# Kernel optimization log

Hardware: AMD Instinct MI355X
Metric: run time of the kernel (lower is better)

## Reference

```python
import jax, jax.numpy as jnp
import numpy as np
from jax import lax

B, DIM, H, W = 4, 256, 32, 32
NH = 8
HD = DIM // NH            # 32; CDA uses doubled head dim 2*HD=64
HIDDEN = 512              # FFN hidden, multiple of DIM (groups=DIM dwconv)
DEPTH = 1
LAMBDA_INIT = 0.8 - 0.6 * float(np.exp(-0.3 * DEPTH))
EPS = 1e-5


def conv1x1(w, x):
    # w: (out,in), x: (b,in,h,w)
    return jnp.einsum('oi,bihw->bohw', w, x)


def dwconv(x, w, groups):
    return lax.conv_general_dilated(x, w, (1, 1), 'SAME',
                                    dimension_numbers=('NCHW', 'OIHW', 'NCHW'),
                                    feature_group_count=groups)


def layernorm_c(x, wgt, bias):
    # WithBias LayerNorm over channel dim (to_3d -> LN(-1) -> to_4d)
    mu = jnp.mean(x, axis=1, keepdims=True)
    var = jnp.mean((x - mu) ** 2, axis=1, keepdims=True)
    return (x - mu) / jnp.sqrt(var + EPS) * wgt[None, :, None, None] + bias[None, :, None, None]


def batchnorm(x, g, b, m, v):
    return (x - m[None, :, None, None]) / jnp.sqrt(v[None, :, None, None] + EPS) \
        * g[None, :, None, None] + b[None, :, None, None]


def _cda(x, wq, wk, wv, lq1, lk1, lq2, lk2, rms_scale, wo):
    b, c, hh, ww = x.shape
    n = hh * ww

    def heads(wp):
        t = conv1x1(wp, x).reshape(b, NH, 2 * HD, n)
        return jnp.transpose(t, (0, 1, 3, 2))  # b h n (2hd)

    Q, K, V = heads(wq), heads(wk), heads(wv)
    scale = HD ** -0.5
    a1 = jax.nn.softmax(jnp.einsum('bhnd,bhmd->bhnm', Q[..., :HD], K[..., :HD]) * scale, axis=-1)
    a2 = jax.nn.softmax(jnp.einsum('bhnd,bhmd->bhnm', Q[..., HD:], K[..., HD:]) * scale, axis=-1)
    lam = jnp.exp(jnp.sum(lq1 * lk1, -1)) - jnp.exp(jnp.sum(lq2 * lk2, -1)) + LAMBDA_INIT  # (NH,)
    out = jnp.einsum('bhnm,bhmd->bhnd', a1 - lam[None, :, None, None] * a2, V)
    rms = jnp.sqrt(jnp.mean(out * out, axis=-1, keepdims=True) + EPS)
    out = out / rms * rms_scale * (1.0 - LAMBDA_INIT)
    out = jnp.transpose(out, (0, 1, 3, 2)).reshape(b, 2 * c, hh, ww)
    return conv1x1(wo, out)


def _cha(x, temp, wqkv, wdw, wout):
    b, c, hh, ww = x.shape
    n = hh * ww
    qkv = dwconv(conv1x1(wqkv, x), wdw, 3 * DIM)
    r = qkv.reshape(b, 3, NH, c // NH, n)
    q, k, v = r[:, 0], r[:, 1], r[:, 2]
    q = q / jnp.maximum(jnp.linalg.norm(q, axis=-1, keepdims=True), 1e-12)
    k = k / jnp.maximum(jnp.linalg.norm(k, axis=-1, keepdims=True), 1e-12)
    attn = jax.nn.softmax(jnp.einsum('bhcn,bhdn->bhcd', q, k) * temp[None, :, None, None], axis=-1)
    out = jnp.einsum('bhcd,bhdn->bhcn', attn, v).reshape(b, c, hh, ww)
    return conv1x1(wout, out)


def _ffn(x, bn1_g, bn1_b, bn1_m, bn1_v, w1, b1, bn2_g, bn2_b, bn2_m, bn2_v, w2, b2, w3, b3):
    h = batchnorm(x, bn1_g, bn1_b, bn1_m, bn1_v)
    h = conv1x1(w1, h) + b1[None, :, None, None]
    h = batchnorm(h, bn2_g, bn2_b, bn2_m, bn2_v)
    h = dwconv(h, w2, DIM) + b2[None, :, None, None]
    h = jnp.clip(h, 0.0, 6.0)  # ReLU6
    return conv1x1(w3, h) + b3[None, :, None, None]


def setup_inputs() -> dict:
    key = jax.random.key(0)
    ks = jax.random.split(key, 20)
    nrm = lambda i, shape, s=0.02: jax.random.normal(ks[i], shape, jnp.float32) * s
    return {
        'x': jax.random.normal(ks[0], (B, DIM, H, W), jnp.float32),
        'ln1_w': jnp.ones((DIM,), jnp.float32), 'ln1_b': jnp.zeros((DIM,), jnp.float32),
        'cda_wq': nrm(1, (2 * DIM, DIM)), 'cda_wk': nrm(2, (2 * DIM, DIM)), 'cda_wv': nrm(3, (2 * DIM, DIM)),
        'cda_lq1': nrm(4, (NH, HD), 0.1), 'cda_lk1': nrm(5, (NH, HD), 0.1),
        'cda_lq2': nrm(6, (NH, HD), 0.1), 'cda_lk2': nrm(7, (NH, HD), 0.1),
        'cda_rms_scale': jnp.ones((2 * HD,), jnp.float32), 'cda_wo': nrm(8, (DIM, 2 * DIM)),
        'ln2_w': jnp.ones((DIM,), jnp.float32), 'ln2_b': jnp.zeros((DIM,), jnp.float32),
        'cha_temp': jnp.ones((NH,), jnp.float32),
        'cha_wqkv': nrm(9, (3 * DIM, DIM)), 'cha_wdw': nrm(10, (3 * DIM, 1, 3, 3), 0.1),
        'cha_wout': nrm(11, (DIM, DIM)),
        'ln3_w': jnp.ones((DIM,), jnp.float32), 'ln3_b': jnp.zeros((DIM,), jnp.float32),
        'bn1_g': jnp.ones((DIM,), jnp.float32), 'bn1_b': jnp.zeros((DIM,), jnp.float32),
        'bn1_m': nrm(12, (DIM,), 0.1), 'bn1_v': jnp.ones((DIM,), jnp.float32),
        'ffn_w1': nrm(13, (HIDDEN, DIM)), 'ffn_b1': jnp.zeros((HIDDEN,), jnp.float32),
        'bn2_g': jnp.ones((HIDDEN,), jnp.float32), 'bn2_b': jnp.zeros((HIDDEN,), jnp.float32),
        'bn2_m': nrm(14, (HIDDEN,), 0.1), 'bn2_v': jnp.ones((HIDDEN,), jnp.float32),
        'ffn_w2': nrm(15, (HIDDEN, HIDDEN // DIM, 3, 3), 0.1), 'ffn_b2': jnp.zeros((HIDDEN,), jnp.float32),
        'ffn_w3': nrm(16, (DIM, HIDDEN)), 'ffn_b3': jnp.zeros((DIM,), jnp.float32),
    }


def reference(x, ln1_w, ln1_b, cda_wq, cda_wk, cda_wv, cda_lq1, cda_lk1, cda_lq2, cda_lk2,
              cda_rms_scale, cda_wo, ln2_w, ln2_b, cha_temp, cha_wqkv, cha_wdw, cha_wout,
              ln3_w, ln3_b, bn1_g, bn1_b, bn1_m, bn1_v, ffn_w1, ffn_b1, bn2_g, bn2_b,
              bn2_m, bn2_v, ffn_w2, ffn_b2, ffn_w3, ffn_b3):
    h = layernorm_c(x, ln1_w, ln1_b)
    x = x + _cda(h, cda_wq, cda_wk, cda_wv, cda_lq1, cda_lk1, cda_lq2, cda_lk2, cda_rms_scale, cda_wo)
    h = layernorm_c(x, ln2_w, ln2_b)
    x = x + _cha(h, cha_temp, cha_wqkv, cha_wdw, cha_wout)
    h = layernorm_c(x, ln3_w, ln3_b)
    x = x + _ffn(h, bn1_g, bn1_b, bn1_m, bn1_v, ffn_w1, ffn_b1, bn2_g, bn2_b, bn2_m, bn2_v, ffn_w2, ffn_b2, ffn_w3, ffn_b3)
    return x
```

## Files before the change

kernel.cpp:

```cpp
#include <hip/hip_runtime.h>
#include <hip/hip_bf16.h>

typedef __hip_bfloat16 bf16;
typedef __attribute__((ext_vector_type(8))) short s16x8;
typedef __attribute__((ext_vector_type(4))) float f32x4;

#define DEV __device__ __forceinline__

DEV float b2f(bf16 v){ return __bfloat162float(v); }
DEV ushort f2bf(float f){ bf16 h = __float2bfloat16(f); return *reinterpret_cast<ushort*>(&h); }

constexpr int NPIX = 1024;
constexpr float EPSF = 1e-5f;
constexpr float LAMBDA_INIT_F = 0.3555090675909693f;
constexpr float ONE_M_LI     = 0.6444909324090307f;
constexpr float ATT_SCALE    = 0.17677669529663687f;

constexpr size_t OFF_WBF   = 2120448;
constexpr size_t OFF_QT    = 2644736;
constexpr size_t OFF_V16   = 4741888;
constexpr size_t OFF_ATT   = 5790464;
constexpr size_t OFF_BUF1  = 6839040;
constexpr size_t OFF_BUF2  = 9984768;
constexpr size_t OFF_SPART = 13130496;
constexpr size_t OFF_STATS = 13425408;
constexpr size_t OFF_EFF   = 13449984;
constexpr size_t OFF_FLAG  = 13452608;

struct PackArgs { const void* p[34]; };

__global__ __launch_bounds__(256) void detect_kernel(const void* __restrict__ x, int* __restrict__ flag){
  __shared__ int sh;
  if (threadIdx.x == 0) sh = 0;
  __syncthreads();
  const bf16* h = (const bf16*)x;
  int local = 0;
  for (int i = threadIdx.x; i < 4096; i += 256){
    float v = b2f(h[i]);
    if (!(fabsf(v) <= 1e6f)) local = 1;
  }
  if (local) atomicOr(&sh, 1);
  __syncthreads();
  if (threadIdx.x == 0) *flag = sh;
}

DEV float rdin(const PackArgs& a, int i, int idx, int flag){
  return flag ? ((const float*)a.p[i])[idx] : b2f(((const bf16*)a.p[i])[idx]);
}

__global__ __launch_bounds__(256) void prep_all_kernel(PackArgs args, const int* __restrict__ flagp,
    float* __restrict__ P, ushort* __restrict__ W, float* __restrict__ eff){
  const int t = threadIdx.x;
  const int blk = blockIdx.x;
  const int flag = *flagp;
  if (blk < 8283){
    constexpr int NIN = 34;
    constexpr int off[NIN+1] = {0,1048576,1048832,1049088,1180160,1311232,1442304,1442560,
      1442816,1443072,1443328,1443392,1574464,1574720,1574976,1574984,1771592,1778504,
      1844040,1844296,1844552,1844808,1845064,1845320,1845576,1976648,1977160,1977672,
      1978184,1978696,1979208,1988424,1988936,2120008,2120264};
    const int g = blk*256 + t;
    if (g >= off[NIN]) return;
    int idx = 0;
    #pragma unroll
    for (int k = 1; k < NIN; k++) idx = (g >= off[k]) ? k : idx;
    P[g] = rdin(args, idx, g - off[idx], flag);
  } else if (blk < 9307){
    const int g = (blk - 8283)*1024 + t*4;
    int src, loc;
    if      (g <  131072){ src = 3;  loc = g; }
    else if (g <  262144){ src = 4;  loc = g - 131072; }
    else if (g <  393216){ src = 5;  loc = g - 262144; }
    else if (g <  589824){ src = 15; loc = g - 393216; }
    else if (g <  720896){ src = 11; loc = g - 589824; }
    else if (g <  786432){ src = 17; loc = g - 720896; }
    else if (g <  917504){ src = 24; loc = g - 786432; }
    else                 { src = 32; loc = g - 917504; }
    ushort4 o;
    if (flag){
      const float4 v = *(const float4*)((const float*)args.p[src] + loc);
      o = make_ushort4(f2bf(v.x), f2bf(v.y), f2bf(v.z), f2bf(v.w));
    } else {
      o = *(const ushort4*)((const ushort*)args.p[src] + loc);
    }
    *(ushort4*)&W[g] = o;
  } else {
    eff[t]      = rdin(args,1,t,flag);  eff[256+t] = rdin(args,2,t,flag);
    eff[512+t]  = rdin(args,12,t,flag); eff[768+t] = rdin(args,13,t,flag);
    const float s1 = rdin(args,20,t,flag) * rsqrtf(rdin(args,23,t,flag) + EPSF);
    eff[1024+t] = rdin(args,18,t,flag) * s1;
    eff[1280+t] = (rdin(args,19,t,flag) - rdin(args,22,t,flag)) * s1 + rdin(args,21,t,flag);
    for (int c = t; c < 512; c += 256){
      const float sc = rdin(args,26,c,flag) * rsqrtf(rdin(args,29,c,flag) + EPSF);
      eff[1536+c] = sc;
      eff[2048+c] = rdin(args,27,c,flag) - rdin(args,28,c,flag)*sc;
    }
    if (t < 8){
      float e1 = 0.f, e2 = 0.f;
      for (int i = 0; i < 32; i++){
        e1 += rdin(args,6,t*32+i,flag) * rdin(args,7,t*32+i,flag);
        e2 += rdin(args,8,t*32+i,flag) * rdin(args,9,t*32+i,flag);
      }
      eff[2560+t] = __expf(e1) - __expf(e2) + LAMBDA_INIT_F;
    }
  }
}

__global__ __launch_bounds__(256) void ln_stats_kernel(const float* __restrict__ x,
    float* __restrict__ mu, float* __restrict__ rstd){
  __shared__ float ps[16][64], ps2[16][64];
  const int t = threadIdx.x;
  const int b = blockIdx.x >> 4, n0 = (blockIdx.x & 15)*64;
  const int tn = t & 15, tc = t >> 4;
  float4 s = {0,0,0,0}, q = {0,0,0,0};
  #pragma unroll
  for (int i = 0; i < 16; i++){
    const int c = tc*16 + i;
    const float4 v = *(const float4*)&x[((size_t)b*256 + c)*NPIX + n0 + tn*4];
    s.x += v.x; s.y += v.y; s.z += v.z; s.w += v.w;
    q.x += v.x*v.x; q.y += v.y*v.y; q.z += v.z*v.z; q.w += v.w*v.w;
  }
  ps[tc][tn*4+0]=s.x; ps[tc][tn*4+1]=s.y; ps[tc][tn*4+2]=s.z; ps[tc][tn*4+3]=s.w;
  ps2[tc][tn*4+0]=q.x; ps2[tc][tn*4+1]=q.y; ps2[tc][tn*4+2]=q.z; ps2[tc][tn*4+3]=q.w;
  __syncthreads();
  if (t < 64){
    float a = 0.f, qq = 0.f;
    #pragma unroll
    for (int j = 0; j < 16; j++){ a += ps[j][t]; qq += ps2[j][t]; }
    const float m = a * (1.f/256.f);
    float var = qq * (1.f/256.f) - m*m; var = fmaxf(var, 0.f);
    mu[(size_t)b*NPIX + n0 + t] = m;
    rstd[(size_t)b*NPIX + n0 + t] = rsqrtf(var + EPSF);
  }
}

template<int INM, int EPIM, bool BIAS, bool BN2F>
__global__ __launch_bounds__(256) void gemm_kernel(
    const float* __restrict__ Xf, const ushort* __restrict__ Xb, const ushort* __restrict__ W,
    const float* __restrict__ bias, const float* __restrict__ mu, const float* __restrict__ rstd,
    const float* __restrict__ effw, const float* __restrict__ effb,
    const float* __restrict__ s2, const float* __restrict__ t2,
    const float* __restrict__ res, void* __restrict__ out,
    ushort* __restrict__ qt, ushort* __restrict__ v16,
    int Cin, const int* __restrict__ flag)
{
  __shared__ ushort Xt[64][72];
  const int t = threadIdx.x;
  const int nb = blockIdx.x*64, ob = blockIdx.y*64, b = blockIdx.z;
  const int lane = t & 63, w = t >> 6;
  const int wR = w >> 1, wC = w & 1;
  const int l15 = lane & 15, g = lane >> 4;
  const int tn = t & 63, tc4 = t >> 6;
  const f32x4 z4 = {0.f,0.f,0.f,0.f};
  f32x4 acc[2][2] = {{z4,z4},{z4,z4}};

  for (int kb = 0; kb < Cin; kb += 64){
    if (INM == 2){
      const ushort* src = Xb + ((size_t)b*NPIX + nb + tn)*Cin + kb + tc4*16;
      *(uint4*)&Xt[tn][tc4*16]   = *(const uint4*)src;
      *(uint4*)&Xt[tn][tc4*16+8] = *(const uint4*)(src+8);
    } else {
      float m_ = 0.f, r_ = 1.f;
      if (INM == 0){ m_ = mu[(size_t)b*NPIX + nb + tn]; r_ = rstd[(size_t)b*NPIX + nb + tn]; }
      ushort tmp[16];
      #pragma unroll
      for (int i = 0; i < 16; i++){
        const int c = kb + tc4*16 + i;
        float v = Xf[((size_t)b*Cin + c)*NPIX + nb + tn];
        if (INM == 0) v = (v - m_)*r_*effw[c] + effb[c];
        tmp[i] = f2bf(v);
      }
      *(uint4*)&Xt[tn][tc4*16]   = *(uint4*)&tmp[0];
      *(uint4*)&Xt[tn][tc4*16+8] = *(uint4*)&tmp[8];
    }
    __syncthreads();
    #pragma unroll
    for (int ks = 0; ks < 2; ks++){
      const s16x8 a0 = *(const s16x8*)&W[(size_t)(ob + wR*32 + l15)*Cin + kb + ks*32 + g*8];
      const s16x8 a1 = *(const s16x8*)&W[(size_t)(ob + wR*32 + 16 + l15)*Cin + kb + ks*32 + g*8];
      const s16x8 b0 = *(const s16x8*)&Xt[wC*32 + l15][ks*32 + g*8];
      const s16x8 b1 = *(const s16x8*)&Xt[wC*32 + 16 + l15][ks*32 + g*8];
      acc[0][0] = __builtin_amdgcn_mfma_f32_16x16x32_bf16(a0, b0, acc[0][0], 0,0,0);
      acc[0][1] = __builtin_amdgcn_mfma_f32_16x16x32_bf16(a0, b1, acc[0][1], 0,0,0);
      acc[1][0] = __builtin_amdgcn_mfma_f32_16x16x32_bf16(a1, b0, acc[1][0], 0,0,0);
      acc[1][1] = __builtin_amdgcn_mfma_f32_16x16x32_bf16(a1, b1, acc[1][1], 0,0,0);
    }
    __syncthreads();
  }

  const int Cout = gridDim.y*64;
  #pragma unroll
  for (int fr = 0; fr < 2; fr++){
    #pragma unroll
    for (int fc = 0; fc < 2; fc++){
      const int o = ob + wR*32 + fr*16 + 4*g;
      const int n = nb + wC*32 + fc*16 + l15;
      const f32x4 v = acc[fr][fc];
      if (EPIM == 0){
        if (ob < 1024){
          const int qk = o >> 9, h = (o >> 6) & 7, d = o & 63;
          ushort4 pk = make_ushort4(f2bf(v[0]), f2bf(v[1]), f2bf(v[2]), f2bf(v[3]));
          ushort* dst = qt + ((((size_t)qk*4 + b)*8 + h)*NPIX + n)*64 + d;
          *(ushort4*)dst = pk;
        } else {
          const int c = o - 1024;
          #pragma unroll
          for (int r = 0; r < 4; r++)
            v16[((size_t)b*512 + c + r)*NPIX + n] = f2bf(v[r]);
        }
      } else {
        #pragma unroll
        for (int r = 0; r < 4; r++){
          float val = v[r];
          if (BIAS) val += bias[o + r];
          if (BN2F) val = val*s2[o+r] + t2[o+r];
          const size_t row = ((size_t)b*Cout + o + r)*NPIX + n;
          if (EPIM == 1){ ((float*)out)[row] = val + res[row]; }
          else if (EPIM == 2){ ((float*)out)[row] = val; }
          else {
            val += res[row];
            if (*flag) ((float*)out)[row] = val;
            else       ((ushort*)out)[row] = f2bf(val);
          }
        }
      }
    }
  }
}

__global__ __launch_bounds__(256) void attn_kernel(
    const ushort* __restrict__ QT, const ushort* __restrict__ V16,
    const float* __restrict__ Pf, const float* __restrict__ lamArr,
    ushort* __restrict__ att)
{
  __shared__ ushort Ks[2][4096];
  __shared__ ushort Vs[2][4096];
  const int t = threadIdx.x;
  const int lane = t & 63, w = t >> 6;
  const int l15 = lane & 15, g = lane >> 4;
  const int qt = blockIdx.x, h = blockIdx.y, b = blockIdx.z;
  const int qsub = qt*64 + w*16;
  const ushort* Qb = QT + ((size_t)b*8 + h)*NPIX*64;
  const ushort* Kb = QT + ((size_t)(4 + b)*8 + h)*NPIX*64;
  const ushort* Vb = V16 + ((size_t)b*512 + h*64)*NPIX;

  const int c0row = t >> 3, c0col = t & 7;
  const int c1row = (t + 256) >> 3, c1col = t & 7;
  const int sw0 = (c0col ^ (c0row & 7))*8;
  const int sw1 = (c1col ^ (c1row & 7))*8;

  s16x8 bq[2];
  #pragma unroll
  for (int hx = 0; hx < 2; hx++)
    bq[hx] = *(const s16x8*)&Qb[(size_t)(qsub + l15)*64 + 32*hx + 8*g];
  const float lam = lamArr[h];

  const f32x4 z4 = {0.f,0.f,0.f,0.f};
  f32x4 o0[4] = {z4,z4,z4,z4};
  f32x4 o1[4] = {z4,z4,z4,z4};
  float z[2] = {0.f, 0.f};

  uint4 kra = *(const uint4*)&Kb[(size_t)c0row*64 + c0col*8];
  uint4 krb = *(const uint4*)&Kb[(size_t)c1row*64 + c1col*8];
  uint4 vra = *(const uint4*)&Vb[(size_t)c0row*NPIX + c0col*8];
  uint4 vrb = *(const uint4*)&Vb[(size_t)c1row*NPIX + c1col*8];
  *(uint4*)&Ks[0][c0row*64 + sw0] = kra;
  *(uint4*)&Ks[0][c1row*64 + sw1] = krb;
  *(uint4*)&Vs[0][c0row*64 + sw0] = vra;
  *(uint4*)&Vs[0][c1row*64 + sw1] = vrb;
  kra = *(const uint4*)&Kb[(size_t)(64 + c0row)*64 + c0col*8];
  krb = *(const uint4*)&Kb[(size_t)(64 + c1row)*64 + c1col*8];
  vra = *(const uint4*)&Vb[(size_t)c0row*NPIX + 64 + c0col*8];
  vrb = *(const uint4*)&Vb[(size_t)c1row*NPIX + 64 + c1col*8];
  __syncthreads();

  #pragma unroll 1
  for (int it = 0; it < 16; it++){
    const int cur = it & 1;
    const ushort* Kc = &Ks[cur][0];
    const ushort* Vc = &Vs[cur][0];

    f32x4 s[2][4];
    #pragma unroll
    for (int fr = 0; fr < 4; fr++){
      const int row = fr*16 + l15;
      const int rx = (row & 7)*8;
      #pragma unroll
      for (int hx = 0; hx < 2; hx++){
        const s16x8 ak = *(const s16x8*)&Kc[row*64 + ((hx*32 + 8*g) ^ rx)];
        s[hx][fr] = __builtin_amdgcn_mfma_f32_16x16x32_bf16(ak, bq[hx], z4, 0,0,0);
      }
    }
    s16x8 pa[2][2];
    #pragma unroll
    for (int hx = 0; hx < 2; hx++){
      #pragma unroll
      for (int ms = 0; ms < 2; ms++){
        ushort tmp[8];
        #pragma unroll
        for (int fr2 = 0; fr2 < 2; fr2++)
          #pragma unroll
          for (int r = 0; r < 4; r++){
            const float e = __expf(s[hx][ms*2 + fr2][r] * ATT_SCALE);
            z[hx] += e;
            tmp[fr2*4 + r] = f2bf(e);
          }
        pa[hx][ms] = *(s16x8*)tmp;
      }
    }
    __builtin_amdgcn_s_setprio(1);
    #pragma unroll
    for (int ms = 0; ms < 2; ms++){
      #pragma unroll
      for (int dc = 0; dc < 4; dc++){
        const int row = dc*16 + l15;
        const int r7 = row & 7;
        const int elo = ms*32 + 4*g;
        const int eloswz = ((((elo >> 3) ^ r7) << 3) | (elo & 7));
        const int ehi = elo + 16;
        const int ehiswz = ((((ehi >> 3) ^ r7) << 3) | (ehi & 7));
        const uint2 lo = *(const uint2*)&Vc[row*64 + eloswz];
        const uint2 hi = *(const uint2*)&Vc[row*64 + ehiswz];
        union { uint u[4]; s16x8 v; } bv;
        bv.u[0] = lo.x; bv.u[1] = lo.y; bv.u[2] = hi.x; bv.u[3] = hi.y;
        o0[dc] = __builtin_amdgcn_mfma_f32_16x16x32_bf16(pa[0][ms], bv.v, o0[dc], 0,0,0);
        o1[dc] = __builtin_amdgcn_mfma_f32_16x16x32_bf16(pa[1][ms], bv.v, o1[dc], 0,0,0);
      }
    }
    __builtin_amdgcn_s_setprio(0);

    if (it < 15){
      const int nxt = cur ^ 1;
      *(uint4*)&Ks[nxt][c0row*64 + sw0] = kra;
      *(uint4*)&Ks[nxt][c1row*64 + sw1] = krb;
      *(uint4*)&Vs[nxt][c0row*64 + sw0] = vra;
      *(uint4*)&Vs[nxt][c1row*64 + sw1] = vrb;
      if (it < 14){
        const int m0 = (it + 2)*64;
        kra = *(const uint4*)&Kb[(size_t)(m0 + c0row)*64 + c0col*8];
        krb = *(const uint4*)&Kb[(size_t)(m0 + c1row)*64 + c1col*8];
        vra = *(const uint4*)&Vb[(size_t)c0row*NPIX + m0 + c0col*8];
        vrb = *(const uint4*)&Vb[(size_t)c1row*NPIX + m0 + c1col*8];
      }
    }
    __syncthreads();
  }

  #pragma unroll
  for (int hx = 0; hx < 2; hx++){
    z[hx] += __shfl_xor(z[hx], 16);
    z[hx] += __shfl_xor(z[hx], 32);
  }
  float zi0[4], zi1[4];
  #pragma unroll
  for (int r = 0; r < 4; r++){
    zi0[r] = 1.f / __shfl(z[0], 4*g + r);
    zi1[r] = 1.f / __shfl(z[1], 4*g + r);
  }
  float val[4][4];
  float ss[4] = {0.f,0.f,0.f,0.f};
  #pragma unroll
  for (int dc = 0; dc < 4; dc++)
    #pragma unroll
    for (int r = 0; r < 4; r++){
      const float vv = o0[dc][r]*zi0[r] - lam*o1[dc][r]*zi1[r];
      val[dc][r] = vv; ss[r] += vv*vv;
    }
  #pragma unroll
  for (int r = 0; r < 4; r++){
    ss[r] += __shfl_xor(ss[r], 1);
    ss[r] += __shfl_xor(ss[r], 2);
    ss[r] += __shfl_xor(ss[r], 4);
    ss[r] += __shfl_xor(ss[r], 8);
  }
  float rinv[4];
  #pragma unroll
  for (int r = 0; r < 4; r++) rinv[r] = ONE_M_LI * rsqrtf(ss[r]*(1.f/64.f) + EPSF);
  #pragma unroll
  for (int dc = 0; dc < 4; dc++){
    const float rs = Pf[1443328 + dc*16 + l15];
    #pragma unroll
    for (int r = 0; r < 4; r++){
      const int n = qsub + 4*g + r;
      att[((size_t)b*NPIX + n)*512 + h*64 + dc*16 + l15] = f2bf(val[dc][r]*rinv[r]*rs);
    }
  }
}

__global__ __launch_bounds__(256) void dwl2_kernel(const float* __restrict__ in,
    const float* __restrict__ wdw, float* __restrict__ out){
  __shared__ float tile[1024];
  __shared__ float wsum[4];
  const int p = blockIdx.x;
  const int c = p % 768;
  const int t = threadIdx.x;
  const float* ip = in + (size_t)p*1024;
  *(float4*)&tile[t*4] = *(const float4*)&ip[t*4];
  float wv[9];
  #pragma unroll
  for (int i = 0; i < 9; i++) wv[i] = wdw[c*9+i];
  __syncthreads();
  float o[4]; float ssq = 0.f;
  #pragma unroll
  for (int j = 0; j < 4; j++){
    const int px = t*4 + j, x = px & 31, y = px >> 5;
    float s = 0.f;
    #pragma unroll
    for (int ky = 0; ky < 3; ky++){
      const int yy = y + ky - 1;
      if (yy < 0 || yy > 31) continue;
      #pragma unroll
      for (int kx = 0; kx < 3; kx++){
        const int xx = x + kx - 1;
        if (xx < 0 || xx > 31) continue;
        s = fmaf(tile[yy*32+xx], wv[ky*3+kx], s);
      }
    }
    o[j] = s; ssq += s*s;
  }
  for (int off = 32; off; off >>= 1) ssq += __shfl_down(ssq, off);
  if ((t & 63) == 0) wsum[t >> 6] = ssq;
  __syncthreads();
  float inv = 1.f;
  if (c < 512){
    const float tot = wsum[0]+wsum[1]+wsum[2]+wsum[3];
    inv = 1.f / fmaxf(sqrtf(tot), 1e-12f);
  }
  *(float4*)&out[(size_t)p*1024 + t*4] = make_float4(o[0]*inv, o[1]*inv, o[2]*inv, o[3]*inv);
}

__global__ __launch_bounds__(256) void cha_scores_kernel(const float* __restrict__ qk,
                                                         float* __restrict__ spart){
  __shared__ float qs[32][129];
  __shared__ float ks[32][129];
  const int t = threadIdx.x;
  const int nb = blockIdx.x*128;
  const int bh = blockIdx.y, b = bh >> 3, h = bh & 7;
  const size_t qbase = ((size_t)b*768 + h*32)*NPIX + nb;
  const size_t kbase = qbase + (size_t)256*NPIX;
  { const int c = t >> 3, n0 = (t & 7)*16;
    #pragma unroll
    for (int j = 0; j < 16; j++){
      qs[c][n0+j] = qk[qbase + (size_t)c*NPIX + n0 + j];
      ks[c][n0+j] = qk[kbase + (size_t)c*NPIX + n0 + j];
    } }
  __syncthreads();
  const int c = t & 31, dg = t >> 5;
  float acc[4] = {};
  for (int nn = 0; nn < 128; nn++){
    const float qv = qs[c][nn];
    #pragma unroll
    for (int j = 0; j < 4; j++) acc[j] = fmaf(qv, ks[dg*4+j][nn], acc[j]);
  }
  float* sp = spart + ((size_t)bh*8 + blockIdx.x)*1024 + c*32 + dg*4;
  #pragma unroll
  for (int j = 0; j < 4; j++) sp[j] = acc[j];
}

__global__ __launch_bounds__(256) void cha_pv_kernel(const float* __restrict__ spart,
    const float* __restrict__ tempP, const float* __restrict__ qkv, float* __restrict__ out){
  __shared__ float Ps[32][33];
  const int t = threadIdx.x;
  const int bh = blockIdx.y, b = bh >> 3, h = bh & 7;
  const int nb = blockIdx.x*64;
  const float tf = tempP[h];
  for (int p = t; p < 1024; p += 256){
    float s = 0.f;
    #pragma unroll
    for (int ch = 0; ch < 8; ch++) s += spart[((size_t)bh*8 + ch)*1024 + p];
    Ps[p >> 5][p & 31] = s * tf;
  }
  __syncthreads();
  if (t < 32){
    float mx = -1e30f;
    #pragma unroll
    for (int d = 0; d < 32; d++) mx = fmaxf(mx, Ps[t][d]);
    float sum = 0.f;
    float e[32];
    #pragma unroll
    for (int d = 0; d < 32; d++){ e[d] = __expf(Ps[t][d]-mx); sum += e[d]; }
    const float inv = 1.f/sum;
    #pragma unroll
    for (int d = 0; d < 32; d++) Ps[t][d] = e[d]*inv;
  }
  __syncthreads();
  const int n = nb + (t & 63);
  const int cg = t >> 6;
  const size_t vbase = ((size_t)b*768 + 512 + h*32)*NPIX + n;
  float acc[8] = {};
  for (int d = 0; d < 32; d++){
    const float v = qkv[vbase + (size_t)d*NPIX];
    #pragma unroll
    for (int j = 0; j < 8; j++) acc[j] = fmaf(Ps[cg*8+j][d], v, acc[j]);
  }
  const size_t obase = ((size_t)b*256 + h*32 + cg*8)*NPIX + n;
  #pragma unroll
  for (int j = 0; j < 8; j++) out[obase + (size_t)j*NPIX] = acc[j];
}

__global__ void gconv3_kernel(const float* __restrict__ in, const float* __restrict__ w,
                              const float* __restrict__ bias, float* __restrict__ out){
  const int gIdx = blockIdx.x*256 + threadIdx.x;
  const int x = gIdx & 31, y = (gIdx >> 5) & 31;
  const int plane = gIdx >> 10;
  const int o = plane & 511, b = plane >> 9;
  const float* ip = in + ((size_t)b*512 + (o & ~1))*NPIX;
  float s = bias[o];
  #pragma unroll
  for (int ci = 0; ci < 2; ci++){
    #pragma unroll
    for (int ky = 0; ky < 3; ky++){
      const int yy = y + ky - 1;
      if (yy < 0 || yy > 31) continue;
      #pragma unroll
      for (int kx = 0; kx < 3; kx++){
        const int xx = x + kx - 1;
        if (xx < 0 || xx > 31) continue;
        s = fmaf(ip[(size_t)ci*NPIX + yy*32+xx], w[o*18 + ci*9 + ky*3 + kx], s);
      }
    }
  }
  out[gIdx] = fminf(fmaxf(s, 0.f), 6.f);
}

extern "C" void kernel_launch(void* const* d_in, const int* in_sizes, int n_in,
                              void* d_out, int out_size, void* d_ws, size_t ws_size,
                              hipStream_t stream)
{
  (void)in_sizes; (void)n_in; (void)out_size; (void)ws_size;

  float* ws   = (float*)d_ws;
  float* P    = ws;
  float* xbuf = P;
  ushort* Wbf = (ushort*)(ws + OFF_WBF);
  ushort* QT  = (ushort*)(ws + OFF_QT);
  ushort* V16 = (ushort*)(ws + OFF_V16);
  ushort* att = (ushort*)(ws + OFF_ATT);
  float* chaout = ws + OFF_ATT;
  float* buf1 = ws + OFF_BUF1;
  float* buf2 = ws + OFF_BUF2;
  float* spart= ws + OFF_SPART;
  float* stats= ws + OFF_STATS;
  float* eff  = ws + OFF_EFF;
  int*  flag  = (int*)(ws + OFF_FLAG);

  const float* b1f = P + 1976648;
  const float* b3f = P + 2120008;
  const float* w2f = P + 1979208;
  const float* b2f_ = P + 1988424;
  const float* temp = P + 1574976;

  detect_kernel<<<1, 256, 0, stream>>>(d_in[0], flag);
  PackArgs pa;
  for (int i = 0; i < 34; i++) pa.p[i] = d_in[i];
  prep_all_kernel<<<9308, 256, 0, stream>>>(pa, flag, P, Wbf, eff);

  ln_stats_kernel<<<64, 256, 0, stream>>>(xbuf, stats, stats+4096);
  gemm_kernel<0,0,false,false><<<dim3(16,24,4), 256, 0, stream>>>(
      xbuf, nullptr, Wbf, nullptr, stats, stats+4096, eff, eff+256,
      nullptr, nullptr, nullptr, nullptr, QT, V16, 256, nullptr);
  attn_kernel<<<dim3(16,8,4), 256, 0, stream>>>(QT, V16, P, eff+2560, att);
  gemm_kernel<2,1,false,false><<<dim3(16,4,4), 256, 0, stream>>>(
      nullptr, att, Wbf+589824, nullptr, nullptr, nullptr, nullptr, nullptr,
      nullptr, nullptr, xbuf, xbuf, nullptr, nullptr, 512, nullptr);

  ln_stats_kernel<<<64, 256, 0, stream>>>(xbuf, stats+8192, stats+12288);
  gemm_kernel<0,2,false,false><<<dim3(16,12,4), 256, 0, stream>>>(
      xbuf, nullptr, Wbf+393216, nullptr, stats+8192, stats+12288, eff+512, eff+768,
      nullptr, nullptr, nullptr, buf1, nullptr, nullptr, 256, nullptr);
  dwl2_kernel<<<3072, 256, 0, stream>>>(buf1, P + 1771592, buf2);
  cha_scores_kernel<<<dim3(8,32), 256, 0, stream>>>(buf2, spart);
  cha_pv_kernel<<<dim3(16,32), 256, 0, stream>>>(spart, temp, buf2, chaout);
  gemm_kernel<1,1,false,false><<<dim3(16,4,4), 256, 0, stream>>>(
      chaout, nullptr, Wbf+720896, nullptr, nullptr, nullptr, nullptr, nullptr,
      nullptr, nullptr, xbuf, xbuf, nullptr, nullptr, 256, nullptr);

  ln_stats_kernel<<<64, 256, 0, stream>>>(xbuf, stats+16384, stats+20480);
  gemm_kernel<0,2,true,true><<<dim3(16,8,4), 256, 0, stream>>>(
      xbuf, nullptr, Wbf+786432, b1f, stats+16384, stats+20480, eff+1024, eff+1280,
      eff+1536, eff+2048, nullptr, buf1, nullptr, nullptr, 256, nullptr);
  gconv3_kernel<<<8192, 256, 0, stream>>>(buf1, w2f, b2f_, buf2);
  gemm_kernel<1,3,true,false><<<dim3(16,4,4), 256, 0, stream>>>(
      buf2, nullptr, Wbf+917504, b3f, nullptr, nullptr, nullptr, nullptr,
      nullptr, nullptr, xbuf, d_out, nullptr, nullptr, 512, flag);
}
```

Baseline: 303.9 us.

## Fuse LayerNorm statistics into prep and GEMM epilogues; tile grouped conv in LDS

Removes the three standalone ln_stats launches. The first LN's sums are computed inside prep_all_kernel from the raw input. The later two are accumulated as per-pixel sum and sum-of-squares in the residual GEMM epilogues, via LDS atomics followed by global atomics, and the consuming GEMM turns these sums into mean and rstd. The grouped 3x3 conv is rewritten to stage its two input planes in LDS, with each thread computing four pixels. The cost is atomic contention and float-order nondeterminism. The prep stats path also redundantly reads its input twice.

```diff
diff --git a/kernel.cpp b/kernel.cpp
--- a/kernel.cpp
+++ b/kernel.cpp
@@ -49,7 +49,8 @@
 }
 
 __global__ __launch_bounds__(256) void prep_all_kernel(PackArgs args, const int* __restrict__ flagp,
-    float* __restrict__ P, ushort* __restrict__ W, float* __restrict__ eff){
+    float* __restrict__ P, ushort* __restrict__ W, float* __restrict__ eff, float* __restrict__ stats){
+  __shared__ float ps[16][64], ps2[16][64];
   const int t = threadIdx.x;
   const int blk = blockIdx.x;
   const int flag = *flagp;
@@ -84,7 +85,7 @@
       o = *(const ushort4*)((const ushort*)args.p[src] + loc);
     }
     *(ushort4*)&W[g] = o;
-  } else {
+  } else if (blk == 9307){
     eff[t]      = rdin(args,1,t,flag);  eff[256+t] = rdin(args,2,t,flag);
     eff[512+t]  = rdin(args,12,t,flag); eff[768+t] = rdin(args,13,t,flag);
     const float s1 = rdin(args,20,t,flag) * rsqrtf(rdin(args,23,t,flag) + EPSF);
@@ -103,38 +104,47 @@
       }
       eff[2560+t] = __expf(e1) - __expf(e2) + LAMBDA_INIT_F;
     }
-  }
-}
-
-__global__ __launch_bounds__(256) void ln_stats_kernel(const float* __restrict__ x,
-    float* __restrict__ mu, float* __restrict__ rstd){
-  __shared__ float ps[16][64], ps2[16][64];
-  const int t = threadIdx.x;
-  const int b = blockIdx.x >> 4, n0 = (blockIdx.x & 15)*64;
-  const int tn = t & 15, tc = t >> 4;
-  float4 s = {0,0,0,0}, q = {0,0,0,0};
-  #pragma unroll
-  for (int i = 0; i < 16; i++){
-    const int c = tc*16 + i;
-    const float4 v = *(const float4*)&x[((size_t)b*256 + c)*NPIX + n0 + tn*4];
-    s.x += v.x; s.y += v.y; s.z += v.z; s.w += v.w;
-    q.x += v.x*v.x; q.y += v.y*v.y; q.z += v.z*v.z; q.w += v.w*v.w;
-  }
-  ps[tc][tn*4+0]=s.x; ps[tc][tn*4+1]=s.y; ps[tc][tn*4+2]=s.z; ps[tc][tn*4+3]=s.w;
-  ps2[tc][tn*4+0]=q.x; ps2[tc][tn*4+1]=q.y; ps2[tc][tn*4+2]=q.z; ps2[tc][tn*4+3]=q.w;
-  __syncthreads();
-  if (t < 64){
-    float a = 0.f, qq = 0.f;
-    #pragma unroll
-    for (int j = 0; j < 16; j++){ a += ps[j][t]; qq += ps2[j][t]; }
-    const float m = a * (1.f/256.f);
-    float var = qq * (1.f/256.f) - m*m; var = fmaxf(var, 0.f);
-    mu[(size_t)b*NPIX + n0 + t] = m;
-    rstd[(size_t)b*NPIX + n0 + t] = rsqrtf(var + EPSF);
-  }
-}
-
-template<int INM, int EPIM, bool BIAS, bool BN2F>
+    for (int i = t; i < 16384; i += 256) stats[8192 + i] = 0.f;
+  } else {
+    const int bi = blk - 9308;
+    const int b = bi >> 4, n0 = (bi & 15)*64;
+    const int tn = t & 15, tc = t >> 4;
+    float s = 0.f, q = 0.f;
+    #pragma unroll 4
+    for (int i = 0; i < 16; i++){
+      const int c = tc*16 + i;
+      #pragma unroll
+      for (int j = 0; j < 4; j++){
+        const float v = rdin(args, 0, ((b*256 + c) << 10) + n0 + tn*4 + j, flag);
+        s += v; q += v*v;
+      }
+    }
+    ps[tc][tn*4+0] = 0.f;
+    ps[tc][tn*4] = 0.f;
+    float sj[4] = {0,0,0,0}, qj[4] = {0,0,0,0};
+    #pragma unroll 4
+    for (int i = 0; i < 16; i++){
+      const int c = tc*16 + i;
+      #pragma unroll
+      for (int j = 0; j < 4; j++){
+        const float v = rdin(args, 0, ((b*256 + c) << 10) + n0 + tn*4 + j, flag);
+        sj[j] += v; qj[j] += v*v;
+      }
+    }
+    #pragma unroll
+    for (int j = 0; j < 4; j++){ ps[tc][tn*4+j] = sj[j]; ps2[tc][tn*4+j] = qj[j]; }
+    __syncthreads();
+    if (t < 64){
+      float a = 0.f, qq = 0.f;
+      #pragma unroll
+      for (int j2 = 0; j2 < 16; j2++){ a += ps[j2][t]; qq += ps2[j2][t]; }
+      stats[(size_t)b*NPIX + n0 + t] = a;
+      stats[4096 + (size_t)b*NPIX + n0 + t] = qq;
+    }
+  }
+}
+
+template<int INM, int EPIM, bool BIAS, bool BN2F, bool STATS>
 __global__ __launch_bounds__(256) void gemm_kernel(
     const float* __restrict__ Xf, const ushort* __restrict__ Xb, const ushort* __restrict__ W,
     const float* __restrict__ bias, const float* __restrict__ mu, const float* __restrict__ rstd,
@@ -142,6 +152,7 @@
     const float* __restrict__ s2, const float* __restrict__ t2,
     const float* __restrict__ res, void* __restrict__ out,
     ushort* __restrict__ qt, ushort* __restrict__ v16,
+    float* __restrict__ gstats,
     int Cin, const int* __restrict__ flag)
 {
   __shared__ ushort Xt[64][72];
@@ -161,7 +172,13 @@
       *(uint4*)&Xt[tn][tc4*16+8] = *(const uint4*)(src+8);
     } else {
       float m_ = 0.f, r_ = 1.f;
-      if (INM == 0){ m_ = mu[(size_t)b*NPIX + nb + tn]; r_ = rstd[(size_t)b*NPIX + nb + tn]; }
+      if (INM == 0){
+        const float sv = mu[(size_t)b*NPIX + nb + tn];
+        const float qv = rstd[(size_t)b*NPIX + nb + tn];
+        m_ = sv * (1.f/256.f);
+        const float var = qv*(1.f/256.f) - m_*m_;
+        r_ = rsqrtf(fmaxf(var, 0.f) + EPSF);
+      }
       ushort tmp[16];
       #pragma unroll
       for (int i = 0; i < 16; i++){
@@ -189,6 +206,7 @@
   }
 
   const int Cout = gridDim.y*64;
+  float sst[2] = {0.f, 0.f}, qst[2] = {0.f, 0.f};
   #pragma unroll
   for (int fr = 0; fr < 2; fr++){
     #pragma unroll
@@ -215,7 +233,11 @@
           if (BIAS) val += bias[o + r];
           if (BN2F) val = val*s2[o+r] + t2[o+r];
           const size_t row = ((size_t)b*Cout + o + r)*NPIX + n;
-          if (EPIM == 1){ ((float*)out)[row] = val + res[row]; }
+          if (EPIM == 1){
+            const float vf = val + res[row];
+            ((float*)out)[row] = vf;
+            if (STATS){ sst[fc] += vf; qst[fc] += vf*vf; }
+          }
           else if (EPIM == 2){ ((float*)out)[row] = val; }
           else {
             val += res[row];
@@ -224,6 +246,22 @@
           }
         }
       }
+    }
+  }
+  if (STATS){
+    float* sacc = (float*)&Xt[0][0];
+    if (t < 128) sacc[t] = 0.f;
+    __syncthreads();
+    #pragma unroll
+    for (int fc = 0; fc < 2; fc++){
+      const int nl = wC*32 + fc*16 + l15;
+      atomicAdd(&sacc[nl*2+0], sst[fc]);
+      atomicAdd(&sacc[nl*2+1], qst[fc]);
+    }
+    __syncthreads();
+    if (t < 64){
+      atomicAdd(&gstats[(size_t)b*NPIX + nb + t],        sacc[t*2+0]);
+      atomicAdd(&gstats[4096 + (size_t)b*NPIX + nb + t], sacc[t*2+1]);
     }
   }
 }
@@ -498,29 +536,42 @@
   for (int j = 0; j < 8; j++) out[obase + (size_t)j*NPIX] = acc[j];
 }
 
-__global__ void gconv3_kernel(const float* __restrict__ in, const float* __restrict__ w,
-                              const float* __restrict__ bias, float* __restrict__ out){
-  const int gIdx = blockIdx.x*256 + threadIdx.x;
-  const int x = gIdx & 31, y = (gIdx >> 5) & 31;
-  const int plane = gIdx >> 10;
-  const int o = plane & 511, b = plane >> 9;
-  const float* ip = in + ((size_t)b*512 + (o & ~1))*NPIX;
-  float s = bias[o];
-  #pragma unroll
-  for (int ci = 0; ci < 2; ci++){
-    #pragma unroll
-    for (int ky = 0; ky < 3; ky++){
-      const int yy = y + ky - 1;
-      if (yy < 0 || yy > 31) continue;
-      #pragma unroll
-      for (int kx = 0; kx < 3; kx++){
-        const int xx = x + kx - 1;
-        if (xx < 0 || xx > 31) continue;
-        s = fmaf(ip[(size_t)ci*NPIX + yy*32+xx], w[o*18 + ci*9 + ky*3 + kx], s);
-      }
-    }
-  }
-  out[gIdx] = fminf(fmaxf(s, 0.f), 6.f);
+__global__ __launch_bounds__(256) void gconv_lds_kernel(const float* __restrict__ in,
+    const float* __restrict__ w, const float* __restrict__ bias, float* __restrict__ out){
+  __shared__ float tin[2][1024];
+  const int p = blockIdx.x;
+  const int o = p & 511, b = p >> 9;
+  const int t = threadIdx.x;
+  const float* ip = in + ((size_t)b*512 + (o & ~1))*1024;
+  *(float4*)&tin[0][t*4] = *(const float4*)&ip[t*4];
+  *(float4*)&tin[1][t*4] = *(const float4*)&ip[1024 + t*4];
+  float wv[18];
+  #pragma unroll
+  for (int i = 0; i < 18; i++) wv[i] = w[o*18 + i];
+  const float bs = bias[o];
+  __syncthreads();
+  float res[4];
+  #pragma unroll
+  for (int j = 0; j < 4; j++){
+    const int px = t*4 + j, x = px & 31, y = px >> 5;
+    float s = bs;
+    #pragma unroll
+    for (int ci = 0; ci < 2; ci++){
+      #pragma unroll
+      for (int ky = 0; ky < 3; ky++){
+        const int yy = y + ky - 1;
+        if (yy < 0 || yy > 31) continue;
+        #pragma unroll
+        for (int kx = 0; kx < 3; kx++){
+          const int xx = x + kx - 1;
+          if (xx < 0 || xx > 31) continue;
+          s = fmaf(tin[ci][yy*32+xx], wv[ci*9 + ky*3 + kx], s);
+        }
+      }
+    }
+    res[j] = fminf(fmaxf(s, 0.f), 6.f);
+  }
+  *(float4*)&out[(size_t)p*1024 + t*4] = make_float4(res[0], res[1], res[2], res[3]);
 }
 
 extern "C" void kernel_launch(void* const* d_in, const int* in_sizes, int n_in,
@@ -553,34 +604,31 @@
   detect_kernel<<<1, 256, 0, stream>>>(d_in[0], flag);
   PackArgs pa;
   for (int i = 0; i < 34; i++) pa.p[i] = d_in[i];
-  prep_all_kernel<<<9308, 256, 0, stream>>>(pa, flag, P, Wbf, eff);
-
-  ln_stats_kernel<<<64, 256, 0, stream>>>(xbuf, stats, stats+4096);
-  gemm_kernel<0,0,false,false><<<dim3(16,24,4), 256, 0, stream>>>(
+  prep_all_kernel<<<9372, 256, 0, stream>>>(pa, flag, P, Wbf, eff, stats);
+
+  gemm_kernel<0,0,false,false,false><<<dim3(16,24,4), 256, 0, stream>>>(
       xbuf, nullptr, Wbf, nullptr, stats, stats+4096, eff, eff+256,
-      nullptr, nullptr, nullptr, nullptr, QT, V16, 256, nullptr);
+      nullptr, nullptr, nullptr, nullptr, QT, V16, nullptr, 256, nullptr);
   attn_kernel<<<dim3(16,8,4), 256, 0, stream>>>(QT, V16, P, eff+2560, att);
-  gemm_kernel<2,1,false,false><<<dim3(16,4,4), 256, 0, stream>>>(
+  gemm_kernel<2,1,false,false,true><<<dim3(16,4,4), 256, 0, stream>>>(
       nullptr, att, Wbf+589824, nullptr, nullptr, nullptr, nullptr, nullptr,
-      nullptr, nullptr, xbuf, xbuf, nullptr, nullptr, 512, nullptr);
-
-  ln_stats_kernel<<<64, 256, 0, stream>>>(xbuf, stats+8192, stats+12288);
-  gemm_kernel<0,2,false,false><<<dim3(16,12,4), 256, 0, stream>>>(
+      nullptr, nullptr, xbuf, xbuf, nullptr, nullptr, stats+8192, 512, nullptr);
+
+  gemm_kernel<0,2,false,false,false><<<dim3(16,12,4), 256, 0, stream>>>(
       xbuf, nullptr, Wbf+393216, nullptr, stats+8192, stats+12288, eff+512, eff+768,
-      nullptr, nullptr, nullptr, buf1, nullptr, nullptr, 256, nullptr);
+      nullptr, nullptr, nullptr, buf1, nullptr, nullptr, nullptr, 256, nullptr);
   dwl2_kernel<<<3072, 256, 0, stream>>>(buf1, P + 1771592, buf2);
   cha_scores_kernel<<<dim3(8,32), 256, 0, stream>>>(buf2, spart);
   cha_pv_kernel<<<dim3(16,32), 256, 0, stream>>>(spart, temp, buf2, chaout);
-  gemm_kernel<1,1,false,false><<<dim3(16,4,4), 256, 0, stream>>>(
+  gemm_kernel<1,1,false,false,true><<<dim3(16,4,4), 256, 0, stream>>>(
       chaout, nullptr, Wbf+720896, nullptr, nullptr, nullptr, nullptr, nullptr,
-      nullptr, nullptr, xbuf, xbuf, nullptr, nullptr, 256, nullptr);
-
-  ln_stats_kernel<<<64, 256, 0, stream>>>(xbuf, stats+16384, stats+20480);
-  gemm_kernel<0,2,true,true><<<dim3(16,8,4), 256, 0, stream>>>(
+      nullptr, nullptr, xbuf, xbuf, nullptr, nullptr, stats+16384, 256, nullptr);
+
+  gemm_kernel<0,2,true,true,false><<<dim3(16,8,4), 256, 0, stream>>>(
       xbuf, nullptr, Wbf+786432, b1f, stats+16384, stats+20480, eff+1024, eff+1280,
-      eff+1536, eff+2048, nullptr, buf1, nullptr, nullptr, 256, nullptr);
-  gconv3_kernel<<<8192, 256, 0, stream>>>(buf1, w2f, b2f_, buf2);
-  gemm_kernel<1,3,true,false><<<dim3(16,4,4), 256, 0, stream>>>(
+      eff+1536, eff+2048, nullptr, buf1, nullptr, nullptr, nullptr, 256, nullptr);
+  gconv_lds_kernel<<<2048, 256, 0, stream>>>(buf1, w2f, b2f_, buf2);
+  gemm_kernel<1,3,true,false,false><<<dim3(16,4,4), 256, 0, stream>>>(
       buf2, nullptr, Wbf+917504, b3f, nullptr, nullptr, nullptr, nullptr,
-      nullptr, nullptr, xbuf, d_out, nullptr, nullptr, 512, flag);
-}
+      nullptr, nullptr, xbuf, d_out, nullptr, nullptr, nullptr, 512, flag);
+}
```

After: 285.9 us. 5.9% less time.
